# Optimization experiments

Measured on AMD Instinct MI355X. Metric: run time of the kernel, lower is better.

## Reference

```python
import jax, jax.numpy as jnp
import numpy as np
import math

OMEGA_0 = 30.0
LAYER_SIZES = [3, 256, 256, 256, 256, 3]
N_POINTS = 524288


def _siren_params(key):
    """SIREN initialization matching the original module."""
    keys = jax.random.split(key, len(LAYER_SIZES) - 1)
    params = {}
    for i in range(len(LAYER_SIZES) - 1):
        in_dim, out_dim = LAYER_SIZES[i], LAYER_SIZES[i + 1]
        k = keys[i]
        bound = (1.0 / in_dim) if i == 0 else (math.sqrt(6.0 / in_dim) / OMEGA_0)
        W = jax.random.uniform(k, (out_dim, in_dim), minval=-bound, maxval=bound, dtype=jnp.float32)
        b = jax.random.uniform(k, (out_dim,), minval=-1e-6, maxval=1e-6, dtype=jnp.float32)
        params[f"W{i}"] = W
        params[f"b{i}"] = b
    return params


def setup_inputs() -> dict:
    key = jax.random.key(0)
    kx, kp = jax.random.split(key)
    # coordinates in [-1, 1], typical SIREN input domain
    x = jax.random.uniform(kx, (N_POINTS, 3), minval=-1.0, maxval=1.0, dtype=jnp.float32)
    inp = {"x": x}
    inp.update(_siren_params(kp))
    return inp


def reference(x, W0, b0, W1, b1, W2, b2, W3, b3, W4, b4):
    # First layer: sin(omega_0 * (W0 @ x + b0)), batched over rows of x.
    h = jnp.sin(OMEGA_0 * (jnp.einsum("ni,oi->no", x, W0) + b0))
    # Hidden layers: sin(W @ h + b)
    h = jnp.sin(jnp.einsum("ni,oi->no", h, W1) + b1)
    h = jnp.sin(jnp.einsum("ni,oi->no", h, W2) + b2)
    h = jnp.sin(jnp.einsum("ni,oi->no", h, W3) + b3)
    # Final layer: linear, no activation.
    out = jnp.einsum("ni,oi->no", h, W4) + b4
    return out
```

## Files before the change

### kernel.cpp

```cpp
#include <hip/hip_runtime.h>
#include <stdint.h>


typedef float    f32x4 __attribute__((ext_vector_type(4)));
typedef short    s16x8 __attribute__((ext_vector_type(8)));
typedef uint32_t u32x2 __attribute__((ext_vector_type(2)));
typedef uint32_t u32x4 __attribute__((ext_vector_type(4)));

#define INV2PI 0.15915494309189535f
#define L0SCALE 4.774648292756860f
#define W4OFF 196608

__device__ __forceinline__ uint16_t f32_to_bf16(float f) {
    uint32_t u = __builtin_bit_cast(uint32_t, f);
    u += 0x7FFFu + ((u >> 16) & 1u);
    return (uint16_t)(u >> 16);
}
__device__ __forceinline__ uint32_t pack_bf16x2(float lo, float hi) {
#if __has_builtin(__builtin_amdgcn_cvt_pk_bf16_f32)
    auto v = __builtin_amdgcn_cvt_pk_bf16_f32(lo, hi);
    return __builtin_bit_cast(uint32_t, v);
#else
    uint32_t a = __builtin_bit_cast(uint32_t, lo);
    uint32_t b = __builtin_bit_cast(uint32_t, hi);
    a += 0x7FFFu + ((a >> 16) & 1u);
    b += 0x7FFFu + ((b >> 16) & 1u);
    return (a >> 16) | (b & 0xFFFF0000u);
#endif
}
__device__ __forceinline__ float sin_rev(float r) {
    return __builtin_amdgcn_sinf(r);
}

__global__ void convert_weights(const float* __restrict__ W1,
                                const float* __restrict__ W2,
                                const float* __restrict__ W3,
                                const float* __restrict__ W4,
                                uint16_t* __restrict__ wsb) {
    int u = blockIdx.x * blockDim.x + threadIdx.x;
    if (u < 24576) {
        int n16 = u & 15, q = (u >> 4) & 3, cH = (u >> 6) & 15,
            kc = (u >> 10) & 7, l = u >> 13;
        const float* W = (l == 0) ? W1 : (l == 1) ? W2 : W3;
        const float* src = W + (cH * 16 + n16) * 256 + kc * 32 + q * 8;
        u32x4 pk;
        #pragma unroll
        for (int j2 = 0; j2 < 4; ++j2)
            pk[j2] = pack_bf16x2(src[2 * j2] * INV2PI, src[2 * j2 + 1] * INV2PI);
        *(u32x4*)(wsb + u * 8) = pk;
    } else if (u < 25088) {
        int e = u - 24576;
        int lane = e & 63, kc = e >> 6;
        int n16 = lane & 15, q = lane >> 4;
        u32x4 pk = { 0u, 0u, 0u, 0u };
        if (n16 < 3) {
            const float* src = W4 + n16 * 256 + kc * 32 + q * 8;
            #pragma unroll
            for (int j2 = 0; j2 < 4; ++j2)
                pk[j2] = pack_bf16x2(src[2 * j2], src[2 * j2 + 1]);
        }
        *(u32x4*)(wsb + W4OFF + e * 8) = pk;
    }
}

__global__ __launch_bounds__(256, 3) void siren_main(
    const float* __restrict__ x,
    const float* __restrict__ W0, const float* __restrict__ b0,
    const float* __restrict__ b1, const float* __restrict__ b2,
    const float* __restrict__ b3,
    const float* __restrict__ b4,
    const uint16_t* __restrict__ Wb,
    float* __restrict__ out)
{
    __shared__ uint16_t h_lds[2048 * 8];

    const int tid  = threadIdx.x;
    const int lane = tid & 63;
    const int wid  = tid >> 6;
    const int n16  = lane & 15;
    const int q    = lane >> 4;
    const int p0   = blockIdx.x * 64;

    {
        float xv[4][3];
        #pragma unroll
        for (int rt = 0; rt < 4; ++rt) {
            const float* xp = x + (p0 + rt * 16 + n16) * 3;
            xv[rt][0] = xp[0]; xv[rt][1] = xp[1]; xv[rt][2] = xp[2];
        }
        #pragma unroll
        for (int oo = 0; oo < 2; ++oo) {
            const int octet = wid * 8 + oo * 4 + q;
            const float* w0r = W0 + octet * 24;
            float wv[24];
            #pragma unroll
            for (int i = 0; i < 24; ++i) wv[i] = w0r[i] * L0SCALE;
            float bb[8];
            #pragma unroll
            for (int i = 0; i < 8; ++i) bb[i] = b0[octet * 8 + i] * L0SCALE;
            const int kc0 = octet >> 2, q0 = octet & 3;
            #pragma unroll
            for (int rt = 0; rt < 4; ++rt) {
                u32x4 pk;
                #pragma unroll
                for (int j2 = 0; j2 < 4; ++j2) {
                    float za = wv[(2*j2  )*3+0] * xv[rt][0] +
                               wv[(2*j2  )*3+1] * xv[rt][1] +
                               wv[(2*j2  )*3+2] * xv[rt][2] + bb[2*j2];
                    float zb = wv[(2*j2+1)*3+0] * xv[rt][0] +
                               wv[(2*j2+1)*3+1] * xv[rt][1] +
                               wv[(2*j2+1)*3+2] * xv[rt][2] + bb[2*j2+1];
                    pk[j2] = pack_bf16x2(sin_rev(za), sin_rev(zb));
                }
                *(u32x4*)&h_lds[((kc0 * 4 + rt) * 64 + q0 * 16 + n16) * 8] = pk;
            }
        }
    }
    __syncthreads();

    #pragma unroll
    for (int l = 0; l < 3; ++l) {
        const uint16_t* wsl = Wb + l * 65536;
        const float* bl = (l == 0) ? b1 : (l == 1) ? b2 : b3;

        s16x8 Wbuf[2][2][4];
        #pragma unroll
        for (int kc2 = 0; kc2 < 2; ++kc2)
            #pragma unroll
            for (int t = 0; t < 4; ++t)
                Wbuf[0][kc2][t] = *(const s16x8*)(wsl + ((kc2 * 16 + wid * 4 + t) * 64 + lane) * 8);

        f32x4 acc[4][4];
        #pragma unroll
        for (int t = 0; t < 4; ++t) {
            f32x4 bv = *(const f32x4*)&bl[wid * 64 + t * 16 + q * 4];
            bv *= INV2PI;
            #pragma unroll
            for (int pt = 0; pt < 4; ++pt) acc[t][pt] = bv;
        }

        #pragma unroll
        for (int kp = 0; kp < 4; ++kp) {
            const int cur = kp & 1, nxt = cur ^ 1;
            if (kp < 3) {
                #pragma unroll
                for (int kc2 = 0; kc2 < 2; ++kc2)
                    #pragma unroll
                    for (int t = 0; t < 4; ++t)
                        Wbuf[nxt][kc2][t] = *(const s16x8*)(wsl +
                            (((kp * 2 + 2 + kc2) * 16 + wid * 4 + t) * 64 + lane) * 8);
            }
            #pragma unroll
            for (int kc2 = 0; kc2 < 2; ++kc2) {
                const int kc = kp * 2 + kc2;
                s16x8 hf[4];
                #pragma unroll
                for (int pt = 0; pt < 4; ++pt)
                    hf[pt] = *(const s16x8*)&h_lds[((kc * 4 + pt) * 64 + lane) * 8];
                #pragma unroll
                for (int t = 0; t < 4; ++t)
                    #pragma unroll
                    for (int pt = 0; pt < 4; ++pt)
                        acc[t][pt] = __builtin_amdgcn_mfma_f32_16x16x32_bf16(
                            Wbuf[cur][kc2][t], hf[pt], acc[t][pt], 0, 0, 0);
            }
        }
        __syncthreads();

        uint32_t* hw = (uint32_t*)h_lds;
        #pragma unroll
        for (int t = 0; t < 4; ++t) {
            const int kcp = wid * 2 + (t >> 1);
            const int qp  = (t * 2 + (q >> 1)) & 3;
            #pragma unroll
            for (int pt = 0; pt < 4; ++pt) {
                float s0 = sin_rev(acc[t][pt][0]);
                float s1 = sin_rev(acc[t][pt][1]);
                float s2 = sin_rev(acc[t][pt][2]);
                float s3 = sin_rev(acc[t][pt][3]);
                int base = ((kcp * 4 + pt) * 64 + qp * 16 + n16) * 4 + (q & 1) * 2;
                u32x2 w2 = { pack_bf16x2(s0, s1), pack_bf16x2(s2, s3) };
                *(u32x2*)&hw[base] = w2;
            }
        }
        __syncthreads();
    }

    {
        float bb4 = (n16 < 3) ? b4[n16] : 0.0f;
        f32x4 accF = { bb4, bb4, bb4, bb4 };
        #pragma unroll
        for (int kc = 0; kc < 8; ++kc) {
            s16x8 w4f = *(const s16x8*)(Wb + W4OFF + (kc * 64 + lane) * 8);
            s16x8 af  = *(const s16x8*)&h_lds[((kc * 4 + wid) * 64 + lane) * 8];
            accF = __builtin_amdgcn_mfma_f32_16x16x32_bf16(af, w4f, accF, 0, 0, 0);
        }
        if (n16 < 3) {
            #pragma unroll
            for (int r = 0; r < 4; ++r)
                out[(p0 + wid * 16 + q * 4 + r) * 3 + n16] = accF[r];
        }
    }
}

extern "C" void kernel_launch(void* const* d_in, const int* in_sizes, int n_in,
                              void* d_out, int out_size, void* d_ws, size_t ws_size,
                              hipStream_t stream) {
    const float* x  = (const float*)d_in[0];
    const float* W0 = (const float*)d_in[1];
    const float* b0 = (const float*)d_in[2];
    const float* W1 = (const float*)d_in[3];
    const float* b1 = (const float*)d_in[4];
    const float* W2 = (const float*)d_in[5];
    const float* b2 = (const float*)d_in[6];
    const float* W3 = (const float*)d_in[7];
    const float* b3 = (const float*)d_in[8];
    const float* W4 = (const float*)d_in[9];
    const float* b4 = (const float*)d_in[10];
    float* outp     = (float*)d_out;
    uint16_t* wsb   = (uint16_t*)d_ws;

    hipLaunchKernelGGL(convert_weights, dim3(98), dim3(256), 0, stream,
                       W1, W2, W3, W4, wsb);
    hipLaunchKernelGGL(siren_main, dim3(8192), dim3(256), 0, stream,
                       x, W0, b0, b1, b2, b3, b4, wsb, outp);
}
```

Measured before the change: 298.4 us.

## Double points per block to 128 to reuse weight fragments across more MFMAs

Each block now handles 128 points instead of 64, with twice the LDS activation buffer and an 8-wide point-tile accumulator per wave. Every weight fragment loaded from global memory now feeds twice as many MFMAs, halving weight traffic per point. The grid is halved and launch bounds drop to 2 blocks per CU to make room for the larger register footprint (128 accumulator floats). This risks lower occupancy and less latency hiding.

```diff
diff --git a/kernel.cpp b/kernel.cpp
--- a/kernel.cpp
+++ b/kernel.cpp
@@ -11,11 +11,6 @@
 #define L0SCALE 4.774648292756860f
 #define W4OFF 196608
 
-__device__ __forceinline__ uint16_t f32_to_bf16(float f) {
-    uint32_t u = __builtin_bit_cast(uint32_t, f);
-    u += 0x7FFFu + ((u >> 16) & 1u);
-    return (uint16_t)(u >> 16);
-}
 __device__ __forceinline__ uint32_t pack_bf16x2(float lo, float hi) {
 #if __has_builtin(__builtin_amdgcn_cvt_pk_bf16_f32)
     auto v = __builtin_amdgcn_cvt_pk_bf16_f32(lo, hi);
@@ -63,7 +58,7 @@
     }
 }
 
-__global__ __launch_bounds__(256, 3) void siren_main(
+__global__ __launch_bounds__(256, 2) void siren_main(
     const float* __restrict__ x,
     const float* __restrict__ W0, const float* __restrict__ b0,
     const float* __restrict__ b1, const float* __restrict__ b2,
@@ -72,19 +67,19 @@
     const uint16_t* __restrict__ Wb,
     float* __restrict__ out)
 {
-    __shared__ uint16_t h_lds[2048 * 8];
+    __shared__ uint16_t h_lds[4096 * 8];
 
     const int tid  = threadIdx.x;
     const int lane = tid & 63;
     const int wid  = tid >> 6;
     const int n16  = lane & 15;
     const int q    = lane >> 4;
-    const int p0   = blockIdx.x * 64;
+    const int p0   = blockIdx.x * 128;
 
     {
-        float xv[4][3];
-        #pragma unroll
-        for (int rt = 0; rt < 4; ++rt) {
+        float xv[8][3];
+        #pragma unroll
+        for (int rt = 0; rt < 8; ++rt) {
             const float* xp = x + (p0 + rt * 16 + n16) * 3;
             xv[rt][0] = xp[0]; xv[rt][1] = xp[1]; xv[rt][2] = xp[2];
         }
@@ -100,7 +95,7 @@
             for (int i = 0; i < 8; ++i) bb[i] = b0[octet * 8 + i] * L0SCALE;
             const int kc0 = octet >> 2, q0 = octet & 3;
             #pragma unroll
-            for (int rt = 0; rt < 4; ++rt) {
+            for (int rt = 0; rt < 8; ++rt) {
                 u32x4 pk;
                 #pragma unroll
                 for (int j2 = 0; j2 < 4; ++j2) {
@@ -112,7 +107,7 @@
                                wv[(2*j2+1)*3+2] * xv[rt][2] + bb[2*j2+1];
                     pk[j2] = pack_bf16x2(sin_rev(za), sin_rev(zb));
                 }
-                *(u32x4*)&h_lds[((kc0 * 4 + rt) * 64 + q0 * 16 + n16) * 8] = pk;
+                *(u32x4*)&h_lds[((kc0 * 8 + rt) * 64 + q0 * 16 + n16) * 8] = pk;
             }
         }
     }
@@ -123,46 +118,52 @@
         const uint16_t* wsl = Wb + l * 65536;
         const float* bl = (l == 0) ? b1 : (l == 1) ? b2 : b3;
 
-        s16x8 Wbuf[2][2][4];
-        #pragma unroll
-        for (int kc2 = 0; kc2 < 2; ++kc2)
-            #pragma unroll
-            for (int t = 0; t < 4; ++t)
-                Wbuf[0][kc2][t] = *(const s16x8*)(wsl + ((kc2 * 16 + wid * 4 + t) * 64 + lane) * 8);
-
-        f32x4 acc[4][4];
+        s16x8 Wbuf[2][4];
+        #pragma unroll
+        for (int t = 0; t < 4; ++t)
+            Wbuf[0][t] = *(const s16x8*)(wsl + ((wid * 4 + t) * 64 + lane) * 8);
+
+        f32x4 acc[4][8];
         #pragma unroll
         for (int t = 0; t < 4; ++t) {
             f32x4 bv = *(const f32x4*)&bl[wid * 64 + t * 16 + q * 4];
             bv *= INV2PI;
             #pragma unroll
-            for (int pt = 0; pt < 4; ++pt) acc[t][pt] = bv;
-        }
-
-        #pragma unroll
-        for (int kp = 0; kp < 4; ++kp) {
-            const int cur = kp & 1, nxt = cur ^ 1;
-            if (kp < 3) {
-                #pragma unroll
-                for (int kc2 = 0; kc2 < 2; ++kc2)
-                    #pragma unroll
-                    for (int t = 0; t < 4; ++t)
-                        Wbuf[nxt][kc2][t] = *(const s16x8*)(wsl +
-                            (((kp * 2 + 2 + kc2) * 16 + wid * 4 + t) * 64 + lane) * 8);
-            }
-            #pragma unroll
-            for (int kc2 = 0; kc2 < 2; ++kc2) {
-                const int kc = kp * 2 + kc2;
+            for (int pt = 0; pt < 8; ++pt) acc[t][pt] = bv;
+        }
+
+        #pragma unroll
+        for (int kc = 0; kc < 8; ++kc) {
+            const int cur = kc & 1, nxt = cur ^ 1;
+            if (kc < 7) {
+                #pragma unroll
+                for (int t = 0; t < 4; ++t)
+                    Wbuf[nxt][t] = *(const s16x8*)(wsl +
+                        (((kc + 1) * 16 + wid * 4 + t) * 64 + lane) * 8);
+            }
+            {
                 s16x8 hf[4];
                 #pragma unroll
                 for (int pt = 0; pt < 4; ++pt)
-                    hf[pt] = *(const s16x8*)&h_lds[((kc * 4 + pt) * 64 + lane) * 8];
+                    hf[pt] = *(const s16x8*)&h_lds[((kc * 8 + pt) * 64 + lane) * 8];
                 #pragma unroll
                 for (int t = 0; t < 4; ++t)
                     #pragma unroll
                     for (int pt = 0; pt < 4; ++pt)
                         acc[t][pt] = __builtin_amdgcn_mfma_f32_16x16x32_bf16(
-                            Wbuf[cur][kc2][t], hf[pt], acc[t][pt], 0, 0, 0);
+                            Wbuf[cur][t], hf[pt], acc[t][pt], 0, 0, 0);
+            }
+            {
+                s16x8 hf[4];
+                #pragma unroll
+                for (int pt = 0; pt < 4; ++pt)
+                    hf[pt] = *(const s16x8*)&h_lds[((kc * 8 + 4 + pt) * 64 + lane) * 8];
+                #pragma unroll
+                for (int t = 0; t < 4; ++t)
+                    #pragma unroll
+                    for (int pt = 0; pt < 4; ++pt)
+                        acc[t][4 + pt] = __builtin_amdgcn_mfma_f32_16x16x32_bf16(
+                            Wbuf[cur][t], hf[pt], acc[t][4 + pt], 0, 0, 0);
             }
         }
         __syncthreads();
@@ -173,12 +174,12 @@
             const int kcp = wid * 2 + (t >> 1);
             const int qp  = (t * 2 + (q >> 1)) & 3;
             #pragma unroll
-            for (int pt = 0; pt < 4; ++pt) {
+            for (int pt = 0; pt < 8; ++pt) {
                 float s0 = sin_rev(acc[t][pt][0]);
                 float s1 = sin_rev(acc[t][pt][1]);
                 float s2 = sin_rev(acc[t][pt][2]);
                 float s3 = sin_rev(acc[t][pt][3]);
-                int base = ((kcp * 4 + pt) * 64 + qp * 16 + n16) * 4 + (q & 1) * 2;
+                int base = ((kcp * 8 + pt) * 64 + qp * 16 + n16) * 4 + (q & 1) * 2;
                 u32x2 w2 = { pack_bf16x2(s0, s1), pack_bf16x2(s2, s3) };
                 *(u32x2*)&hw[base] = w2;
             }
@@ -188,17 +189,24 @@
 
     {
         float bb4 = (n16 < 3) ? b4[n16] : 0.0f;
-        f32x4 accF = { bb4, bb4, bb4, bb4 };
+        f32x4 accF[2] = { { bb4, bb4, bb4, bb4 }, { bb4, bb4, bb4, bb4 } };
         #pragma unroll
         for (int kc = 0; kc < 8; ++kc) {
             s16x8 w4f = *(const s16x8*)(Wb + W4OFF + (kc * 64 + lane) * 8);
-            s16x8 af  = *(const s16x8*)&h_lds[((kc * 4 + wid) * 64 + lane) * 8];
-            accF = __builtin_amdgcn_mfma_f32_16x16x32_bf16(af, w4f, accF, 0, 0, 0);
+            #pragma unroll
+            for (int hh = 0; hh < 2; ++hh) {
+                s16x8 af = *(const s16x8*)&h_lds[
+                    ((kc * 8 + wid * 2 + hh) * 64 + lane) * 8];
+                accF[hh] = __builtin_amdgcn_mfma_f32_16x16x32_bf16(
+                    af, w4f, accF[hh], 0, 0, 0);
+            }
         }
         if (n16 < 3) {
             #pragma unroll
-            for (int r = 0; r < 4; ++r)
-                out[(p0 + wid * 16 + q * 4 + r) * 3 + n16] = accF[r];
+            for (int hh = 0; hh < 2; ++hh)
+                #pragma unroll
+                for (int r = 0; r < 4; ++r)
+                    out[(p0 + (wid * 2 + hh) * 16 + q * 4 + r) * 3 + n16] = accF[hh][r];
         }
     }
 }
@@ -222,6 +230,6 @@
 
     hipLaunchKernelGGL(convert_weights, dim3(98), dim3(256), 0, stream,
                        W1, W2, W3, W4, wsb);
-    hipLaunchKernelGGL(siren_main, dim3(8192), dim3(256), 0, stream,
+    hipLaunchKernelGGL(siren_main, dim3(4096), dim3(256), 0, stream,
                        x, W0, b0, b1, b2, b3, b4, wsb, outp);
 }
```

Measured after the change: 278.3 us. -6.7%, faster.
